# Kernel tuning notes

Hardware: AMD Instinct MI355X
Metric: run time of the kernel (lower is better)

Reference implementation:

```python
import jax, jax.numpy as jnp
import numpy as np
from jax import lax

B, S = 256, 512
CHAR_NUM, CLASS_NUM, OUTPUT_NUM, WORD_EMBED, H = 10, 10, 64, 32, 128
EPS = 1e-12


def setup_inputs() -> dict:
    key = jax.random.key(0)
    ks = jax.random.split(key, 16)
    def nrm(k, shape, s=0.05):
        return jax.random.normal(k, shape, dtype=jnp.float32) * s
    return {
        "char_ids": jax.random.randint(ks[0], (B, S), 0, CHAR_NUM),
        "word_ids": jax.random.randint(ks[1], (B, S), 0, CHAR_NUM),
        "subject_ids": jax.random.randint(ks[2], (B, 2), 0, S),
        "emb_char": nrm(ks[3], (CHAR_NUM, OUTPUT_NUM)),
        "emb_word": nrm(ks[4], (CHAR_NUM, WORD_EMBED)),
        "Wwc": nrm(ks[5], (WORD_EMBED, OUTPUT_NUM)),
        "bwc": jnp.zeros((OUTPUT_NUM,), jnp.float32),
        "l1_Wx": nrm(ks[6], (OUTPUT_NUM, 4 * H)),
        "l1_Wh": nrm(ks[7], (H, 4 * H)),
        "l1_b": jnp.zeros((4 * H,), jnp.float32),
        "l2_Wx": nrm(ks[8], (H, 4 * H)),
        "l2_Wh": nrm(ks[9], (H, 4 * H)),
        "l2_b": jnp.zeros((4 * H,), jnp.float32),
        "beta_W": nrm(ks[10], (2 * H, H)),
        "beta_b": jnp.zeros((H,), jnp.float32),
        "gamma_W": nrm(ks[11], (2 * H, H)),
        "gamma_b": jnp.zeros((H,), jnp.float32),
        "sub_W": nrm(ks[12], (H, 2)),
        "sub_b": jnp.zeros((2,), jnp.float32),
        "po_W": nrm(ks[13], (H, 2 * CLASS_NUM)),
        "po_b": jnp.zeros((2 * CLASS_NUM,), jnp.float32),
    }


def _lstm_cell(x, h, c, Wx, Wh, b):
    # Keras LSTMCell: gates ordered i, f, g(cell), o
    z = x @ Wx + h @ Wh + b
    i, f, g, o = jnp.split(z, 4, axis=-1)
    c_new = jax.nn.sigmoid(f) * c + jax.nn.sigmoid(i) * jnp.tanh(g)
    h_new = jax.nn.sigmoid(o) * jnp.tanh(c_new)
    return h_new, c_new


def reference(char_ids, word_ids, subject_ids,
              emb_char, emb_word, Wwc, bwc,
              l1_Wx, l1_Wh, l1_b, l2_Wx, l2_Wh, l2_b,
              beta_W, beta_b, gamma_W, gamma_b,
              sub_W, sub_b, po_W, po_b):
    b, s = char_ids.shape
    # NOTE: source passes mask = (char_ids == 0) to the RNN; in Keras, mask True
    # means the step IS processed, so only positions with id==0 update state.
    step_mask = (char_ids == 0)  # [B, S] bool

    emb = emb_char[char_ids] + (emb_word[word_ids] @ Wwc + bwc)  # [B, S, 64]

    def step(carry, inp):
        h1, c1, h2, c2 = carry
        xt, mt = inp  # xt [B, 64], mt [B]
        h1n, c1n = _lstm_cell(xt, h1, c1, l1_Wx, l1_Wh, l1_b)
        h2n, c2n = _lstm_cell(h1n, h2, c2, l2_Wx, l2_Wh, l2_b)
        m = mt[:, None]
        h1 = jnp.where(m, h1n, h1)
        c1 = jnp.where(m, c1n, c1)
        h2 = jnp.where(m, h2n, h2)
        c2 = jnp.where(m, c2n, c2)
        return (h1, c1, h2, c2), h2

    z = jnp.zeros((b, H), emb.dtype)
    _, outs = lax.scan(step, (z, z, z, z),
                       (emb.transpose(1, 0, 2), step_mask.T))
    sent = outs.transpose(1, 0, 2)  # [B, S, 128]

    # vectorized batch_gather (replaces eager numpy per-row loop)
    bidx = jnp.arange(b)
    sub_start = sent[bidx, subject_ids[:, 0]]  # [B, 128]
    sub_end = sent[bidx, subject_ids[:, 1]]    # [B, 128]
    subject = jnp.concatenate([sub_start, sub_end], axis=1)  # [B, 256]

    # conditional layer norm
    beta = subject @ beta_W + beta_b    # [B, 128]
    gamma = subject @ gamma_W + gamma_b
    u = jnp.mean(sent, axis=-1, keepdims=True)
    v = jnp.mean((sent - u) ** 2, axis=-1, keepdims=True)
    xhat = (sent - u) / jnp.sqrt(v + EPS)
    context = gamma[:, None, :] * xhat + beta[:, None, :]  # [B, S, 128]

    # (transformer_encoder LSTM(32) output is dead code in the source; omitted)
    sub_preds = sent @ sub_W + sub_b                     # [B, S, 2]
    po_preds = (context @ po_W + po_b).reshape(b, -1, CLASS_NUM, 2)  # [B, S, 10, 2]
    return sub_preds, po_preds
```

## Files before the change

kernel.cpp:

```cpp
#include <hip/hip_runtime.h>
#include <cstdint>
#include <cstddef>


#define SLOTS 192

typedef _Float16 f16x2 __attribute__((ext_vector_type(2)));

__device__ __forceinline__ f16x2 as_h2(unsigned int v) {
    union { unsigned int u; f16x2 h; } x; x.u = v; return x.h;
}

#if __has_builtin(__builtin_amdgcn_fdot2)
__device__ __forceinline__ float fdot2(f16x2 a, f16x2 b, float c) {
    return __builtin_amdgcn_fdot2(a, b, c, false);
}
#else
__device__ __forceinline__ float fdot2(f16x2 a, f16x2 b, float c) {
    return c + (float)a.x * (float)b.x + (float)a.y * (float)b.y;
}
#endif

__device__ __forceinline__ float fast_rcp(float x) {
#if __has_builtin(__builtin_amdgcn_rcpf)
    return __builtin_amdgcn_rcpf(x);
#else
    return 1.f / x;
#endif
}
__device__ __forceinline__ float sigm(float x) {
    x = fminf(fmaxf(x, -30.f), 30.f);
    return fast_rcp(1.f + __expf(-x));
}
__device__ __forceinline__ float tanh_fast(float x) {
    x = fminf(fmaxf(x, -15.f), 15.f);
    float e = __expf(-2.f * x);
    return (1.f - e) * fast_rcp(1.f + e);
}

__device__ __forceinline__ float dpp_bfly4(float v) {
    union { float f; int i; } a, b;
    a.f = v;
    b.i = __builtin_amdgcn_update_dpp(0, a.i, 0xB1, 0xf, 0xf, true);
    a.f += b.f;
    b.i = __builtin_amdgcn_update_dpp(0, a.i, 0x4E, 0xf, 0xf, true);
    a.f += b.f;
    return a.f;
}

__device__ __forceinline__ float dot_u4(float s, const uint4 h, const uint4 w) {
    s = fdot2(as_h2(h.x), as_h2(w.x), s);
    s = fdot2(as_h2(h.y), as_h2(w.y), s);
    s = fdot2(as_h2(h.z), as_h2(w.z), s);
    s = fdot2(as_h2(h.w), as_h2(w.w), s);
    return s;
}

__global__ void k_xw1(const float* __restrict__ emb_char,
                      const float* __restrict__ emb_word,
                      const float* __restrict__ Wwc,
                      const float* __restrict__ bwc,
                      const float* __restrict__ l1_Wx,
                      const float* __restrict__ l1_b,
                      float* __restrict__ XW1) {
    __shared__ float xw[64];
    const int w = blockIdx.x;
    const int T = threadIdx.x;
    if (T < 64) {
        float acc = emb_char[T] + bwc[T];
        for (int m = 0; m < 32; ++m) acc += emb_word[w * 32 + m] * Wwc[m * 64 + T];
        xw[T] = acc;
    }
    __syncthreads();
    float acc = l1_b[T];
    for (int k = 0; k < 64; ++k) acc += xw[k] * l1_Wx[k * 512 + T];
    XW1[w * 512 + T] = acc;
}

__global__ void k_pack2(const float* __restrict__ l1_Wh,
                        const float* __restrict__ l2_Wx,
                        const float* __restrict__ l2_Wh,
                        uint4* __restrict__ W1H, uint4* __restrict__ W2H) {
    const int gid = blockIdx.x * blockDim.x + threadIdx.x;
    union { uint4 qv; f16x2 h[4]; } out;
    if (gid < 8192) {
        const int t = gid >> 4, i = gid & 15;
        const int q = t & 3, u = t >> 2;
        const int j = i >> 2, m = i & 3;
        const int col = u + 128 * j;
        for (int e = 0; e < 4; ++e) {
            const int k = 32 * q + 2 * (4 * m + e);
            f16x2 p;
            p.x = (_Float16)l1_Wh[k * 512 + col];
            p.y = (_Float16)l1_Wh[(k + 1) * 512 + col];
            out.h[e] = p;
        }
        W1H[gid] = out.qv;
    } else {
        const int gid2 = gid - 8192;
        const int t = gid2 >> 5, i = gid2 & 31;
        const int q = t & 3, u = t >> 2;
        const int ph = i >> 4, jm = i & 15;
        const int j = jm >> 2, m = jm & 3;
        const int col = u + 128 * j;
        const float* __restrict__ src = ph ? l2_Wx : l2_Wh;
        for (int e = 0; e < 4; ++e) {
            const int k = 32 * q + 2 * (4 * m + e);
            f16x2 p;
            p.x = (_Float16)src[k * 512 + col];
            p.y = (_Float16)src[(k + 1) * 512 + col];
            out.h[e] = p;
        }
        W2H[gid2] = out.qv;
    }
}

__global__ __launch_bounds__(512, 2) void k_lstm(
    const int* __restrict__ char_ids, const int* __restrict__ word_ids,
    const float* __restrict__ XW1, const uint4* __restrict__ W1H,
    const uint4* __restrict__ W2H, const float* __restrict__ l2_b,
    float* __restrict__ hbuf, unsigned short* __restrict__ idxbuf)
{
    const int b    = blockIdx.x;
    const int T    = threadIdx.x;
    const int lane = T & 63;
    const int wv   = T >> 6;
    const int q    = T & 3;
    const int u    = T >> 2;

    __shared__ int   charL[512];
    __shared__ int   wordL[512];
    __shared__ float XW1L[5120];
    __shared__ __align__(16) _Float16 h1f[2][128];
    __shared__ __align__(16) _Float16 h2f[2][128];
    __shared__ short actT[512];
    __shared__ int   ccnt[8];

    charL[T] = char_ids[b * 512 + T];
    wordL[T] = word_ids[b * 512 + T];
#pragma unroll
    for (int i = 0; i < 10; ++i) XW1L[i * 512 + T] = XW1[i * 512 + T];
    __syncthreads();

    const bool act = (charL[T] == 0);
    const unsigned long long bmask = __ballot(act);
    if (lane == 0) ccnt[wv] = (int)__popcll(bmask);
    __syncthreads();
    int base = 0;
    for (int i = 0; i < wv; ++i) base += ccnt[i];
    int tot = base;
    for (int i = wv; i < 8; ++i) tot += ccnt[i];
    if (act) actT[base + (int)__popcll(bmask & ((1ull << lane) - 1ull))] = (short)T;
    {
        int cin = base + (int)__popcll(bmask & ((2ull << lane) - 1ull));
        idxbuf[b * 512 + T] = (unsigned short)(cin < SLOTS - 1 ? cin : SLOTS - 1);
    }
    const int nact = tot;

    if (T < 128) {
        h1f[0][T] = (_Float16)0.f;
        h1f[1][T] = (_Float16)0.f;
        h2f[0][T] = (_Float16)0.f;
        h2f[1][T] = (_Float16)0.f;
        hbuf[(size_t)b * SLOTS * 128 + T] = 0.f;
    }
    float c1 = 0.f, c2 = 0.f;
    const float l2b0 = l2_b[u];
    const float l2b1 = l2_b[128 + u];
    const float l2b2 = l2_b[256 + u];
    const float l2b3 = l2_b[384 + u];

    uint4 w1[16], w2[32];
    {
        const uint4* W1t = W1H + (size_t)T * 16;
        const uint4* W2t = W2H + (size_t)T * 32;
#pragma unroll
        for (int i = 0; i < 16; ++i) w1[i] = W1t[i];
#pragma unroll
        for (int i = 0; i < 32; ++i) w2[i] = W2t[i];
    }
#pragma unroll
    for (int i = 0; i < 16; ++i)
        asm volatile("" : "+v"(w1[i].x), "+v"(w1[i].y), "+v"(w1[i].z), "+v"(w1[i].w));
#pragma unroll
    for (int i = 0; i < 32; ++i)
        asm volatile("" : "+v"(w2[i].x), "+v"(w2[i].y), "+v"(w2[i].z), "+v"(w2[i].w));

    __syncthreads();

    if (nact > 0) {
        const int w0_ = wordL[actT[0]];
        const float zi = XW1L[w0_ * 512 + u];
        const float zg = XW1L[w0_ * 512 + 256 + u];
        const float zo = XW1L[w0_ * 512 + 384 + u];
        c1 = sigm(zi) * tanh_fast(zg);
        const float h1n = sigm(zo) * tanh_fast(c1);
        if (q == 0) h1f[0][u] = (_Float16)h1n;
        __syncthreads();
    }

#define LSTM_STEP(H1S, H2S, H1D, H2D)                                          \
    {                                                                          \
        const uint4* h1r = (const uint4*)&H1S[0] + 4 * q;                      \
        const uint4 a0 = h1r[0], a1 = h1r[1], a2 = h1r[2], a3 = h1r[3];        \
        const uint4* h2r = (const uint4*)&H2S[0] + 4 * q;                      \
        const uint4 g0 = h2r[0], g1 = h2r[1], g2 = h2r[2], g3 = h2r[3];        \
        const bool more = (a + 1 < nact);                                      \
        const int wid = more ? wordL[actT[a + 1]] : 0;                         \
        const float xwi = XW1L[wid * 512 + u];                                 \
        const float xwf = XW1L[wid * 512 + 128 + u];                           \
        const float xwg = XW1L[wid * 512 + 256 + u];                           \
        const float xwo = XW1L[wid * 512 + 384 + u];                           \
        float p[4];                                                            \
        _Pragma("unroll")                                                      \
        for (int j = 0; j < 4; ++j) {                                          \
            float s = dot_u4(0.f, g0, w2[4 * j + 0]);                          \
            s = dot_u4(s, g1, w2[4 * j + 1]);                                  \
            s = dot_u4(s, g2, w2[4 * j + 2]);                                  \
            s = dot_u4(s, g3, w2[4 * j + 3]);                                  \
            s = dot_u4(s, a0, w2[16 + 4 * j + 0]);                             \
            s = dot_u4(s, a1, w2[16 + 4 * j + 1]);                             \
            s = dot_u4(s, a2, w2[16 + 4 * j + 2]);                             \
            s = dot_u4(s, a3, w2[16 + 4 * j + 3]);                             \
            p[j] = s;                                                          \
        }                                                                      \
        const float y0 = dpp_bfly4(p[0]) + l2b0;                               \
        const float y1 = dpp_bfly4(p[1]) + l2b1;                               \
        const float y2 = dpp_bfly4(p[2]) + l2b2;                               \
        const float y3 = dpp_bfly4(p[3]) + l2b3;                               \
        c2 = sigm(y1) * c2 + sigm(y0) * tanh_fast(y2);                         \
        const float h2v = sigm(y3) * tanh_fast(c2);                            \
        if (q == 0) {                                                          \
            H2D[u] = (_Float16)h2v;                                            \
            const int slot = (a + 1 < SLOTS - 1) ? a + 1 : SLOTS - 1;          \
            hbuf[((size_t)b * SLOTS + slot) * 128 + u] = h2v;                  \
        }                                                                      \
        if (more) {                                                            \
            float r0, r1, r2, r3;                                              \
            {                                                                  \
                float r = dot_u4(0.f, a0, w1[0]);                              \
                r = dot_u4(r, a1, w1[1]);                                      \
                r = dot_u4(r, a2, w1[2]);                                      \
                r = dot_u4(r, a3, w1[3]);                                      \
                r0 = r;                                                        \
                r = dot_u4(0.f, a0, w1[4]);                                    \
                r = dot_u4(r, a1, w1[5]);                                      \
                r = dot_u4(r, a2, w1[6]);                                      \
                r = dot_u4(r, a3, w1[7]);                                      \
                r1 = r;                                                        \
                r = dot_u4(0.f, a0, w1[8]);                                    \
                r = dot_u4(r, a1, w1[9]);                                      \
                r = dot_u4(r, a2, w1[10]);                                     \
                r = dot_u4(r, a3, w1[11]);                                     \
                r2 = r;                                                        \
                r = dot_u4(0.f, a0, w1[12]);                                   \
                r = dot_u4(r, a1, w1[13]);                                     \
                r = dot_u4(r, a2, w1[14]);                                     \
                r = dot_u4(r, a3, w1[15]);                                     \
                r3 = r;                                                        \
            }                                                                  \
            const float zi = dpp_bfly4(r0) + xwi;                              \
            const float zf = dpp_bfly4(r1) + xwf;                              \
            const float zg = dpp_bfly4(r2) + xwg;                              \
            const float zo = dpp_bfly4(r3) + xwo;                              \
            c1 = sigm(zf) * c1 + sigm(zi) * tanh_fast(zg);                     \
            const float h1n = sigm(zo) * tanh_fast(c1);                        \
            if (q == 0) H1D[u] = (_Float16)h1n;                                \
        }                                                                      \
        __syncthreads();                                                       \
    }

    int a = 0;
    while (a < nact) {
        LSTM_STEP(h1f[0], h2f[0], h1f[1], h2f[1]);
        ++a;
        if (a >= nact) break;
        LSTM_STEP(h1f[1], h2f[1], h1f[0], h2f[0]);
        ++a;
    }
#undef LSTM_STEP
}

__global__ __launch_bounds__(256) void k_subject(
    const int* __restrict__ subject_ids,
    const unsigned short* __restrict__ idxbuf,
    const float* __restrict__ hbuf,
    const float* __restrict__ beta_W, const float* __restrict__ beta_b,
    const float* __restrict__ gamma_W, const float* __restrict__ gamma_b,
    float* __restrict__ betaO, float* __restrict__ gammaO)
{
    const int b = blockIdx.x;
    const int T = threadIdx.x;
    const int u = T & 127, half = T >> 7;
    __shared__ float subj[256];
    const int s0 = subject_ids[b * 2 + 0];
    const int s1 = subject_ids[b * 2 + 1];
    const int i0 = idxbuf[b * 512 + s0];
    const int i1 = idxbuf[b * 512 + s1];
    const int slot = half ? i1 : i0;
    subj[T] = hbuf[((size_t)b * SLOTS + slot) * 128 + u];
    __syncthreads();
    const float* __restrict__ W = half ? gamma_W : beta_W;
    float acc = half ? gamma_b[u] : beta_b[u];
    for (int c = 0; c < 256; ++c) acc += subj[c] * W[c * 128 + u];
    if (half) gammaO[b * 128 + u] = acc;
    else      betaO[b * 128 + u]  = acc;
}

__global__ __launch_bounds__(256) void k_out2(
    const unsigned short* __restrict__ idxbuf, const float* __restrict__ hbuf,
    const float* __restrict__ betaO, const float* __restrict__ gammaO,
    const float* __restrict__ sub_W, const float* __restrict__ sub_b,
    const float* __restrict__ po_W, const float* __restrict__ po_b,
    float* __restrict__ out)
{
    const int b = blockIdx.x;
    const int T = threadIdx.x;
    __shared__ float A[20][132];
    __shared__ float K1[20], K2[20];
    __shared__ float gm[128], bt[128];
    __shared__ float urs[192][2];
    __shared__ float povals[192 * 20];
    __shared__ float subv[192 * 2];
    __shared__ unsigned short idxr[512];
    __shared__ float swl[256];

    if (T < 128) { gm[T] = gammaO[b * 128 + T]; bt[T] = betaO[b * 128 + T]; }
    idxr[T] = idxbuf[b * 512 + T];
    idxr[256 + T] = idxbuf[b * 512 + 256 + T];
    swl[T] = sub_W[T];
    __syncthreads();

    for (int i = T; i < 2560; i += 256) {
        const int o = i >> 7, c = i & 127;
        A[o][c] = gm[c] * po_W[c * 20 + o];
    }
    if (T < 20) {
        float k1 = po_b[T], k2 = 0.f;
        for (int c = 0; c < 128; ++c) {
            const float pw = po_W[c * 20 + T];
            k1 += bt[c] * pw;
            k2 += gm[c] * pw;
        }
        K1[T] = k1; K2[T] = k2;
    }
    const int nslot = (int)idxr[511] + 1;
    const float sb0 = sub_b[0], sb1 = sub_b[1];
    for (int s = T; s < nslot; s += 256) {
        const float4* hp4 = (const float4*)(hbuf + ((size_t)b * SLOTS + s) * 128);
        float sum = 0.f, s2 = 0.f, sub0 = sb0, sub1 = sb1;
        for (int c4 = 0; c4 < 32; ++c4) {
            const float4 h = hp4[c4];
            sum += (h.x + h.y) + (h.z + h.w);
            s2  += h.x * h.x + h.y * h.y + h.z * h.z + h.w * h.w;
            const int c = 4 * c4;
            sub0 += h.x * swl[2 * c] + h.y * swl[2 * c + 2] + h.z * swl[2 * c + 4] + h.w * swl[2 * c + 6];
            sub1 += h.x * swl[2 * c + 1] + h.y * swl[2 * c + 3] + h.z * swl[2 * c + 5] + h.w * swl[2 * c + 7];
        }
        const float u = sum * (1.f / 128.f);
        const float v = fmaxf(s2 * (1.f / 128.f) - u * u, 0.f);
        urs[s][0] = u;
        urs[s][1] = 1.f / sqrtf(v + 1e-12f);
        subv[2 * s] = sub0; subv[2 * s + 1] = sub1;
    }
    __syncthreads();

    for (int i = T; i < nslot * 20; i += 256) {
        const int s = i / 20, o = i - 20 * s;
        const float u = urs[s][0], rs = urs[s][1];
        const float4* hp4 = (const float4*)(hbuf + ((size_t)b * SLOTS + s) * 128);
        const float* Ao = &A[o][0];
        float acc = 0.f;
        for (int c4 = 0; c4 < 32; ++c4) {
            const float4 h = hp4[c4];
            const float4 aa = *(const float4*)&Ao[4 * c4];
            acc += h.x * aa.x + h.y * aa.y + h.z * aa.z + h.w * aa.w;
        }
        povals[i] = rs * acc - u * rs * K2[o] + K1[o];
    }
    __syncthreads();

    for (int i = T; i < 2560; i += 256) {
        const int t = i / 5, j = i - 5 * t;
        const int sl = idxr[t];
        const float4 v = *(const float4*)&povals[sl * 20 + 4 * j];
        *(float4*)&out[262144 + ((size_t)(b * 512 + t)) * 20 + 4 * j] = v;
    }
    for (int i = T; i < 512; i += 256) {
        const int sl = idxr[i];
        float2 v; v.x = subv[2 * sl]; v.y = subv[2 * sl + 1];
        *(float2*)&out[((size_t)(b * 512 + i)) * 2] = v;
    }
}

extern "C" void kernel_launch(void* const* d_in, const int* in_sizes, int n_in,
                              void* d_out, int out_size, void* d_ws, size_t ws_size,
                              hipStream_t stream) {
    (void)in_sizes; (void)n_in; (void)out_size; (void)ws_size;
    const int*   char_ids    = (const int*)d_in[0];
    const int*   word_ids    = (const int*)d_in[1];
    const int*   subject_ids = (const int*)d_in[2];
    const float* emb_char    = (const float*)d_in[3];
    const float* emb_word    = (const float*)d_in[4];
    const float* Wwc         = (const float*)d_in[5];
    const float* bwc         = (const float*)d_in[6];
    const float* l1_Wx       = (const float*)d_in[7];
    const float* l1_Wh       = (const float*)d_in[8];
    const float* l1_b        = (const float*)d_in[9];
    const float* l2_Wx       = (const float*)d_in[10];
    const float* l2_Wh       = (const float*)d_in[11];
    const float* l2_b        = (const float*)d_in[12];
    const float* beta_W      = (const float*)d_in[13];
    const float* beta_b      = (const float*)d_in[14];
    const float* gamma_W     = (const float*)d_in[15];
    const float* gamma_b     = (const float*)d_in[16];
    const float* sub_W       = (const float*)d_in[17];
    const float* sub_b       = (const float*)d_in[18];
    const float* po_W        = (const float*)d_in[19];
    const float* po_b        = (const float*)d_in[20];
    float* out = (float*)d_out;

    char* ws = (char*)d_ws;
    float*          XW1    = (float*)(ws + 0);
    uint4*          W1H    = (uint4*)(ws + 32768);
    uint4*          W2H    = (uint4*)(ws + 163840);
    float*          betaO  = (float*)(ws + 425984);
    float*          gammaO = (float*)(ws + 557056);
    unsigned short* idxbuf = (unsigned short*)(ws + 688128);
    float*          hbuf   = (float*)(ws + 950272);

    k_xw1<<<dim3(10), dim3(512), 0, stream>>>(emb_char, emb_word, Wwc, bwc, l1_Wx, l1_b, XW1);
    k_pack2<<<dim3(96), dim3(256), 0, stream>>>(l1_Wh, l2_Wx, l2_Wh, W1H, W2H);
    k_lstm<<<dim3(256), dim3(512), 0, stream>>>(char_ids, word_ids, XW1, W1H, W2H,
                                                l2_b, hbuf, idxbuf);
    k_subject<<<dim3(256), dim3(256), 0, stream>>>(subject_ids, idxbuf, hbuf,
                                                   beta_W, beta_b, gamma_W, gamma_b,
                                                   betaO, gammaO);
    k_out2<<<dim3(256), dim3(256), 0, stream>>>(idxbuf, hbuf, betaO, gammaO,
                                                sub_W, sub_b, po_W, po_b, out);
}
```

Baseline: 244.7 us.

## Split LSTM gate dot products across 8 lanes per unit and fuse small kernels

Each hidden unit's recurrent dot products are now split over 8 threads instead of 4. The LSTM block grows to 1024 threads with half the weight registers per thread, and an extra DPP stage finishes the reduction. This shortens the serial per-step dependency chain at the cost of more threads, more sync participants and an extra shuffle stage. The prep kernels (XW1 table and weight packing) are merged into one launch, the subject/beta-gamma kernel is folded into the output kernel, and word ids are precompacted into a list to cut launch overhead and an indirect lookup.

```diff
diff --git a/kernel.cpp b/kernel.cpp
--- a/kernel.cpp
+++ b/kernel.cpp
@@ -38,13 +38,15 @@
     return (1.f - e) * fast_rcp(1.f + e);
 }
 
-__device__ __forceinline__ float dpp_bfly4(float v) {
+__device__ __forceinline__ float dpp_bfly8(float v) {
     union { float f; int i; } a, b;
     a.f = v;
     b.i = __builtin_amdgcn_update_dpp(0, a.i, 0xB1, 0xf, 0xf, true);
     a.f += b.f;
     b.i = __builtin_amdgcn_update_dpp(0, a.i, 0x4E, 0xf, 0xf, true);
     a.f += b.f;
+    b.i = __builtin_amdgcn_update_dpp(0, a.i, 0x141, 0xf, 0xf, true);
+    a.f += b.f;
     return a.f;
 }
 
@@ -56,66 +58,63 @@
     return s;
 }
 
-__global__ void k_xw1(const float* __restrict__ emb_char,
-                      const float* __restrict__ emb_word,
-                      const float* __restrict__ Wwc,
-                      const float* __restrict__ bwc,
-                      const float* __restrict__ l1_Wx,
-                      const float* __restrict__ l1_b,
-                      float* __restrict__ XW1) {
-    __shared__ float xw[64];
-    const int w = blockIdx.x;
+__global__ __launch_bounds__(512) void k_prep(
+    const float* __restrict__ emb_char, const float* __restrict__ emb_word,
+    const float* __restrict__ Wwc, const float* __restrict__ bwc,
+    const float* __restrict__ l1_Wx, const float* __restrict__ l1_b,
+    const float* __restrict__ l1_Wh, const float* __restrict__ l2_Wx,
+    const float* __restrict__ l2_Wh,
+    float* __restrict__ XW1, uint4* __restrict__ W1H, uint4* __restrict__ W2H)
+{
+    const int blk = blockIdx.x;
     const int T = threadIdx.x;
-    if (T < 64) {
-        float acc = emb_char[T] + bwc[T];
-        for (int m = 0; m < 32; ++m) acc += emb_word[w * 32 + m] * Wwc[m * 64 + T];
-        xw[T] = acc;
-    }
-    __syncthreads();
-    float acc = l1_b[T];
-    for (int k = 0; k < 64; ++k) acc += xw[k] * l1_Wx[k * 512 + T];
-    XW1[w * 512 + T] = acc;
-}
-
-__global__ void k_pack2(const float* __restrict__ l1_Wh,
-                        const float* __restrict__ l2_Wx,
-                        const float* __restrict__ l2_Wh,
-                        uint4* __restrict__ W1H, uint4* __restrict__ W2H) {
-    const int gid = blockIdx.x * blockDim.x + threadIdx.x;
-    union { uint4 qv; f16x2 h[4]; } out;
-    if (gid < 8192) {
-        const int t = gid >> 4, i = gid & 15;
-        const int q = t & 3, u = t >> 2;
-        const int j = i >> 2, m = i & 3;
-        const int col = u + 128 * j;
-        for (int e = 0; e < 4; ++e) {
-            const int k = 32 * q + 2 * (4 * m + e);
-            f16x2 p;
-            p.x = (_Float16)l1_Wh[k * 512 + col];
-            p.y = (_Float16)l1_Wh[(k + 1) * 512 + col];
-            out.h[e] = p;
+    if (blk < 10) {
+        __shared__ float xw[64];
+        if (T < 64) {
+            float acc = emb_char[T] + bwc[T];
+            for (int m = 0; m < 32; ++m) acc += emb_word[blk * 32 + m] * Wwc[m * 64 + T];
+            xw[T] = acc;
         }
-        W1H[gid] = out.qv;
+        __syncthreads();
+        float acc = l1_b[T];
+        for (int k = 0; k < 64; ++k) acc += xw[k] * l1_Wx[k * 512 + T];
+        XW1[blk * 512 + T] = acc;
     } else {
-        const int gid2 = gid - 8192;
-        const int t = gid2 >> 5, i = gid2 & 31;
-        const int q = t & 3, u = t >> 2;
-        const int ph = i >> 4, jm = i & 15;
-        const int j = jm >> 2, m = jm & 3;
-        const int col = u + 128 * j;
-        const float* __restrict__ src = ph ? l2_Wx : l2_Wh;
-        for (int e = 0; e < 4; ++e) {
-            const int k = 32 * q + 2 * (4 * m + e);
-            f16x2 p;
-            p.x = (_Float16)src[k * 512 + col];
-            p.y = (_Float16)src[(k + 1) * 512 + col];
-            out.h[e] = p;
+        const int gid = (blk - 10) * 512 + T;
+        union { uint4 qv; f16x2 h[4]; } out;
+        if (gid < 8192) {
+            const int t = gid >> 3, i = gid & 7;
+            const int q = t & 7, u = t >> 3;
+            const int j = i >> 1, m = i & 1;
+            const int col = u + 128 * j;
+            for (int e = 0; e < 4; ++e) {
+                const int k = 16 * q + 2 * (4 * m + e);
+                f16x2 p;
+                p.x = (_Float16)l1_Wh[k * 512 + col];
+                p.y = (_Float16)l1_Wh[(k + 1) * 512 + col];
+                out.h[e] = p;
+            }
+            W1H[gid] = out.qv;
+        } else {
+            const int gid2 = gid - 8192;
+            const int t = gid2 >> 4, i = gid2 & 15;
+            const int q = t & 7, u = t >> 3;
+            const int j = i >> 2, m = i & 3;
+            const int col = u + 128 * j;
+            for (int e = 0; e < 4; ++e) {
+                const int kk = 32 * q + 2 * (4 * m + e);
+                float w0, w1v;
+                if (kk < 128) { w0 = l2_Wh[kk * 512 + col];          w1v = l2_Wh[(kk + 1) * 512 + col]; }
+                else          { w0 = l2_Wx[(kk - 128) * 512 + col]; w1v = l2_Wx[(kk - 127) * 512 + col]; }
+                f16x2 p; p.x = (_Float16)w0; p.y = (_Float16)w1v;
+                out.h[e] = p;
+            }
+            W2H[gid2] = out.qv;
         }
-        W2H[gid2] = out.qv;
-    }
-}
-
-__global__ __launch_bounds__(512, 2) void k_lstm(
+    }
+}
+
+__global__ __launch_bounds__(1024, 4) void k_lstm(
     const int* __restrict__ char_ids, const int* __restrict__ word_ids,
     const float* __restrict__ XW1, const uint4* __restrict__ W1H,
     const uint4* __restrict__ W2H, const float* __restrict__ l2_b,
@@ -125,8 +124,8 @@
     const int T    = threadIdx.x;
     const int lane = T & 63;
     const int wv   = T >> 6;
-    const int q    = T & 3;
-    const int u    = T >> 2;
+    const int q    = T & 7;
+    const int u    = T >> 3;
 
     __shared__ int   charL[512];
     __shared__ int   wordL[512];
@@ -134,25 +133,38 @@
     __shared__ __align__(16) _Float16 h1f[2][128];
     __shared__ __align__(16) _Float16 h2f[2][128];
     __shared__ short actT[512];
+    __shared__ short wlist[512];
     __shared__ int   ccnt[8];
 
-    charL[T] = char_ids[b * 512 + T];
-    wordL[T] = word_ids[b * 512 + T];
-#pragma unroll
-    for (int i = 0; i < 10; ++i) XW1L[i * 512 + T] = XW1[i * 512 + T];
-    __syncthreads();
-
-    const bool act = (charL[T] == 0);
+    if (T < 512) {
+        charL[T] = char_ids[b * 512 + T];
+        wordL[T] = word_ids[b * 512 + T];
+    }
+    XW1L[T]        = XW1[T];
+    XW1L[1024 + T] = XW1[1024 + T];
+    XW1L[2048 + T] = XW1[2048 + T];
+    XW1L[3072 + T] = XW1[3072 + T];
+    XW1L[4096 + T] = XW1[4096 + T];
+    __syncthreads();
+
+    const bool act = (T < 512) && (charL[T] == 0);
     const unsigned long long bmask = __ballot(act);
-    if (lane == 0) ccnt[wv] = (int)__popcll(bmask);
+    if (lane == 0 && wv < 8) ccnt[wv] = (int)__popcll(bmask);
     __syncthreads();
     int base = 0;
-    for (int i = 0; i < wv; ++i) base += ccnt[i];
-    int tot = base;
-    for (int i = wv; i < 8; ++i) tot += ccnt[i];
-    if (act) actT[base + (int)__popcll(bmask & ((1ull << lane) - 1ull))] = (short)T;
     {
-        int cin = base + (int)__popcll(bmask & ((2ull << lane) - 1ull));
+        const int wcap = wv < 8 ? wv : 8;
+        for (int i = 0; i < wcap; ++i) base += ccnt[i];
+    }
+    int tot = 0;
+    for (int i = 0; i < 8; ++i) tot += ccnt[i];
+    if (act) {
+        const int pos = base + (int)__popcll(bmask & ((1ull << lane) - 1ull));
+        actT[pos]  = (short)T;
+        wlist[pos] = (short)wordL[T];
+    }
+    if (T < 512) {
+        const int cin = base + (int)__popcll(bmask & ((2ull << lane) - 1ull));
         idxbuf[b * 512 + T] = (unsigned short)(cin < SLOTS - 1 ? cin : SLOTS - 1);
     }
     const int nact = tot;
@@ -170,26 +182,26 @@
     const float l2b2 = l2_b[256 + u];
     const float l2b3 = l2_b[384 + u];
 
-    uint4 w1[16], w2[32];
+    uint4 w1[8], w2[16];
     {
-        const uint4* W1t = W1H + (size_t)T * 16;
-        const uint4* W2t = W2H + (size_t)T * 32;
+        const uint4* W1t = W1H + (size_t)T * 8;
+        const uint4* W2t = W2H + (size_t)T * 16;
 #pragma unroll
-        for (int i = 0; i < 16; ++i) w1[i] = W1t[i];
+        for (int i = 0; i < 8; ++i) w1[i] = W1t[i];
 #pragma unroll
-        for (int i = 0; i < 32; ++i) w2[i] = W2t[i];
-    }
+        for (int i = 0; i < 16; ++i) w2[i] = W2t[i];
+    }
+#pragma unroll
+    for (int i = 0; i < 8; ++i)
+        asm volatile("" : "+v"(w1[i].x), "+v"(w1[i].y), "+v"(w1[i].z), "+v"(w1[i].w));
 #pragma unroll
     for (int i = 0; i < 16; ++i)
-        asm volatile("" : "+v"(w1[i].x), "+v"(w1[i].y), "+v"(w1[i].z), "+v"(w1[i].w));
-#pragma unroll
-    for (int i = 0; i < 32; ++i)
         asm volatile("" : "+v"(w2[i].x), "+v"(w2[i].y), "+v"(w2[i].z), "+v"(w2[i].w));
 
     __syncthreads();
 
     if (nact > 0) {
-        const int w0_ = wordL[actT[0]];
+        const int w0_ = wlist[0];
         const float zi = XW1L[w0_ * 512 + u];
         const float zg = XW1L[w0_ * 512 + 256 + u];
         const float zo = XW1L[w0_ * 512 + 384 + u];
@@ -201,33 +213,22 @@
 
 #define LSTM_STEP(H1S, H2S, H1D, H2D)                                          \
     {                                                                          \
-        const uint4* h1r = (const uint4*)&H1S[0] + 4 * q;                      \
-        const uint4 a0 = h1r[0], a1 = h1r[1], a2 = h1r[2], a3 = h1r[3];        \
-        const uint4* h2r = (const uint4*)&H2S[0] + 4 * q;                      \
-        const uint4 g0 = h2r[0], g1 = h2r[1], g2 = h2r[2], g3 = h2r[3];        \
-        const bool more = (a + 1 < nact);                                      \
-        const int wid = more ? wordL[actT[a + 1]] : 0;                         \
-        const float xwi = XW1L[wid * 512 + u];                                 \
-        const float xwf = XW1L[wid * 512 + 128 + u];                           \
-        const float xwg = XW1L[wid * 512 + 256 + u];                           \
-        const float xwo = XW1L[wid * 512 + 384 + u];                           \
-        float p[4];                                                            \
-        _Pragma("unroll")                                                      \
-        for (int j = 0; j < 4; ++j) {                                          \
-            float s = dot_u4(0.f, g0, w2[4 * j + 0]);                          \
-            s = dot_u4(s, g1, w2[4 * j + 1]);                                  \
-            s = dot_u4(s, g2, w2[4 * j + 2]);                                  \
-            s = dot_u4(s, g3, w2[4 * j + 3]);                                  \
-            s = dot_u4(s, a0, w2[16 + 4 * j + 0]);                             \
-            s = dot_u4(s, a1, w2[16 + 4 * j + 1]);                             \
-            s = dot_u4(s, a2, w2[16 + 4 * j + 2]);                             \
-            s = dot_u4(s, a3, w2[16 + 4 * j + 3]);                             \
-            p[j] = s;                                                          \
-        }                                                                      \
-        const float y0 = dpp_bfly4(p[0]) + l2b0;                               \
-        const float y1 = dpp_bfly4(p[1]) + l2b1;                               \
-        const float y2 = dpp_bfly4(p[2]) + l2b2;                               \
-        const float y3 = dpp_bfly4(p[3]) + l2b3;                               \
+        const uint4* srcL2 = (q < 4) ? ((const uint4*)&H2S[0] + 4 * q)         \
+                                     : ((const uint4*)&H1S[0] + 4 * (q - 4));  \
+        uint4 sA = srcL2[0], sB = srcL2[1];                                    \
+        float p0 = dot_u4(dot_u4(0.f, sA, w2[0]),  sB, w2[1]);                 \
+        float p1 = dot_u4(dot_u4(0.f, sA, w2[4]),  sB, w2[5]);                 \
+        float p2 = dot_u4(dot_u4(0.f, sA, w2[8]),  sB, w2[9]);                 \
+        float p3 = dot_u4(dot_u4(0.f, sA, w2[12]), sB, w2[13]);                \
+        sA = srcL2[2]; sB = srcL2[3];                                          \
+        p0 = dot_u4(dot_u4(p0, sA, w2[2]),  sB, w2[3]);                        \
+        p1 = dot_u4(dot_u4(p1, sA, w2[6]),  sB, w2[7]);                        \
+        p2 = dot_u4(dot_u4(p2, sA, w2[10]), sB, w2[11]);                       \
+        p3 = dot_u4(dot_u4(p3, sA, w2[14]), sB, w2[15]);                       \
+        const float y0 = dpp_bfly8(p0) + l2b0;                                 \
+        const float y1 = dpp_bfly8(p1) + l2b1;                                 \
+        const float y2 = dpp_bfly8(p2) + l2b2;                                 \
+        const float y3 = dpp_bfly8(p3) + l2b3;                                 \
         c2 = sigm(y1) * c2 + sigm(y0) * tanh_fast(y2);                         \
         const float h2v = sigm(y3) * tanh_fast(c2);                            \
         if (q == 0) {                                                          \
@@ -235,34 +236,18 @@
             const int slot = (a + 1 < SLOTS - 1) ? a + 1 : SLOTS - 1;          \
             hbuf[((size_t)b * SLOTS + slot) * 128 + u] = h2v;                  \
         }                                                                      \
-        if (more) {                                                            \
-            float r0, r1, r2, r3;                                              \
-            {                                                                  \
-                float r = dot_u4(0.f, a0, w1[0]);                              \
-                r = dot_u4(r, a1, w1[1]);                                      \
-                r = dot_u4(r, a2, w1[2]);                                      \
-                r = dot_u4(r, a3, w1[3]);                                      \
-                r0 = r;                                                        \
-                r = dot_u4(0.f, a0, w1[4]);                                    \
-                r = dot_u4(r, a1, w1[5]);                                      \
-                r = dot_u4(r, a2, w1[6]);                                      \
-                r = dot_u4(r, a3, w1[7]);                                      \
-                r1 = r;                                                        \
-                r = dot_u4(0.f, a0, w1[8]);                                    \
-                r = dot_u4(r, a1, w1[9]);                                      \
-                r = dot_u4(r, a2, w1[10]);                                     \
-                r = dot_u4(r, a3, w1[11]);                                     \
-                r2 = r;                                                        \
-                r = dot_u4(0.f, a0, w1[12]);                                   \
-                r = dot_u4(r, a1, w1[13]);                                     \
-                r = dot_u4(r, a2, w1[14]);                                     \
-                r = dot_u4(r, a3, w1[15]);                                     \
-                r3 = r;                                                        \
-            }                                                                  \
-            const float zi = dpp_bfly4(r0) + xwi;                              \
-            const float zf = dpp_bfly4(r1) + xwf;                              \
-            const float zg = dpp_bfly4(r2) + xwg;                              \
-            const float zo = dpp_bfly4(r3) + xwo;                              \
+        if (a + 1 < nact) {                                                    \
+            const int wid = wlist[a + 1];                                      \
+            const uint4* h1s = (const uint4*)&H1S[0] + 2 * q;                  \
+            const uint4 tA = h1s[0], tB = h1s[1];                              \
+            float r0 = dot_u4(dot_u4(0.f, tA, w1[0]), tB, w1[1]);              \
+            float r1 = dot_u4(dot_u4(0.f, tA, w1[2]), tB, w1[3]);              \
+            float r2 = dot_u4(dot_u4(0.f, tA, w1[4]), tB, w1[5]);              \
+            float r3 = dot_u4(dot_u4(0.f, tA, w1[6]), tB, w1[7]);              \
+            const float zi = dpp_bfly8(r0) + XW1L[wid * 512 + u];              \
+            const float zf = dpp_bfly8(r1) + XW1L[wid * 512 + 128 + u];        \
+            const float zg = dpp_bfly8(r2) + XW1L[wid * 512 + 256 + u];        \
+            const float zo = dpp_bfly8(r3) + XW1L[wid * 512 + 384 + u];        \
             c1 = sigm(zf) * c1 + sigm(zi) * tanh_fast(zg);                     \
             const float h1n = sigm(zo) * tanh_fast(c1);                        \
             if (q == 0) H1D[u] = (_Float16)h1n;                                \
@@ -281,35 +266,11 @@
 #undef LSTM_STEP
 }
 
-__global__ __launch_bounds__(256) void k_subject(
+__global__ __launch_bounds__(256) void k_post(
     const int* __restrict__ subject_ids,
-    const unsigned short* __restrict__ idxbuf,
-    const float* __restrict__ hbuf,
+    const unsigned short* __restrict__ idxbuf, const float* __restrict__ hbuf,
     const float* __restrict__ beta_W, const float* __restrict__ beta_b,
     const float* __restrict__ gamma_W, const float* __restrict__ gamma_b,
-    float* __restrict__ betaO, float* __restrict__ gammaO)
-{
-    const int b = blockIdx.x;
-    const int T = threadIdx.x;
-    const int u = T & 127, half = T >> 7;
-    __shared__ float subj[256];
-    const int s0 = subject_ids[b * 2 + 0];
-    const int s1 = subject_ids[b * 2 + 1];
-    const int i0 = idxbuf[b * 512 + s0];
-    const int i1 = idxbuf[b * 512 + s1];
-    const int slot = half ? i1 : i0;
-    subj[T] = hbuf[((size_t)b * SLOTS + slot) * 128 + u];
-    __syncthreads();
-    const float* __restrict__ W = half ? gamma_W : beta_W;
-    float acc = half ? gamma_b[u] : beta_b[u];
-    for (int c = 0; c < 256; ++c) acc += subj[c] * W[c * 128 + u];
-    if (half) gammaO[b * 128 + u] = acc;
-    else      betaO[b * 128 + u]  = acc;
-}
-
-__global__ __launch_bounds__(256) void k_out2(
-    const unsigned short* __restrict__ idxbuf, const float* __restrict__ hbuf,
-    const float* __restrict__ betaO, const float* __restrict__ gammaO,
     const float* __restrict__ sub_W, const float* __restrict__ sub_b,
     const float* __restrict__ po_W, const float* __restrict__ po_b,
     float* __restrict__ out)
@@ -324,11 +285,27 @@
     __shared__ float subv[192 * 2];
     __shared__ unsigned short idxr[512];
     __shared__ float swl[256];
-
-    if (T < 128) { gm[T] = gammaO[b * 128 + T]; bt[T] = betaO[b * 128 + T]; }
+    __shared__ float subj[256];
+
     idxr[T] = idxbuf[b * 512 + T];
     idxr[256 + T] = idxbuf[b * 512 + 256 + T];
     swl[T] = sub_W[T];
+    {
+        const int uu = T & 127, half = T >> 7;
+        const int sidx = subject_ids[b * 2 + half];
+        const int slot = idxbuf[b * 512 + sidx];
+        subj[T] = hbuf[((size_t)b * SLOTS + slot) * 128 + uu];
+    }
+    __syncthreads();
+
+    {
+        const int uu = T & 127, half = T >> 7;
+        const float* __restrict__ W = half ? gamma_W : beta_W;
+        float acc = half ? gamma_b[uu] : beta_b[uu];
+        for (int c = 0; c < 256; ++c) acc += subj[c] * W[c * 128 + uu];
+        if (half) gm[uu] = acc;
+        else      bt[uu] = acc;
+    }
     __syncthreads();
 
     for (int i = T; i < 2560; i += 256) {
@@ -424,18 +401,15 @@
     float*          XW1    = (float*)(ws + 0);
     uint4*          W1H    = (uint4*)(ws + 32768);
     uint4*          W2H    = (uint4*)(ws + 163840);
-    float*          betaO  = (float*)(ws + 425984);
-    float*          gammaO = (float*)(ws + 557056);
     unsigned short* idxbuf = (unsigned short*)(ws + 688128);
     float*          hbuf   = (float*)(ws + 950272);
 
-    k_xw1<<<dim3(10), dim3(512), 0, stream>>>(emb_char, emb_word, Wwc, bwc, l1_Wx, l1_b, XW1);
-    k_pack2<<<dim3(96), dim3(256), 0, stream>>>(l1_Wh, l2_Wx, l2_Wh, W1H, W2H);
-    k_lstm<<<dim3(256), dim3(512), 0, stream>>>(char_ids, word_ids, XW1, W1H, W2H,
-                                                l2_b, hbuf, idxbuf);
-    k_subject<<<dim3(256), dim3(256), 0, stream>>>(subject_ids, idxbuf, hbuf,
-                                                   beta_W, beta_b, gamma_W, gamma_b,
-                                                   betaO, gammaO);
-    k_out2<<<dim3(256), dim3(256), 0, stream>>>(idxbuf, hbuf, betaO, gammaO,
+    k_prep<<<dim3(58), dim3(512), 0, stream>>>(emb_char, emb_word, Wwc, bwc,
+                                               l1_Wx, l1_b, l1_Wh, l2_Wx, l2_Wh,
+                                               XW1, W1H, W2H);
+    k_lstm<<<dim3(256), dim3(1024), 0, stream>>>(char_ids, word_ids, XW1, W1H, W2H,
+                                                 l2_b, hbuf, idxbuf);
+    k_post<<<dim3(256), dim3(256), 0, stream>>>(subject_ids, idxbuf, hbuf,
+                                                beta_W, beta_b, gamma_W, gamma_b,
                                                 sub_W, sub_b, po_W, po_b, out);
 }
```

Measured after the change: 273.5 us. 11.8% more time.

## Fuse subject projection and output head into LSTM kernel using shared-memory history

Applied to the files above, without the earlier changes.

The two small preprocessing kernels are merged into one launch. The subject-projection and output-head kernels are folded into the tail of the LSTM kernel. The per-step h2 history now stays in padded shared memory instead of a global buffer, so it is no longer written and re-read from global memory, and two launches plus their global round trips go away. The trade-off is a much larger shared-memory footprint per block, which may cut blocks per CU. The history capacity also shrinks from 192 to 128 slots, so the last slot clamps if a row has more active steps than that.

```diff
diff --git a/kernel.cpp b/kernel.cpp
--- a/kernel.cpp
+++ b/kernel.cpp
@@ -3,7 +3,8 @@
 #include <cstddef>
 
 
-#define SLOTS 192
+#define HIST 128
+#define HPAD 132
 
 typedef _Float16 f16x2 __attribute__((ext_vector_type(2)));
 
@@ -56,70 +57,73 @@
     return s;
 }
 
-__global__ void k_xw1(const float* __restrict__ emb_char,
-                      const float* __restrict__ emb_word,
-                      const float* __restrict__ Wwc,
-                      const float* __restrict__ bwc,
-                      const float* __restrict__ l1_Wx,
-                      const float* __restrict__ l1_b,
-                      float* __restrict__ XW1) {
-    __shared__ float xw[64];
-    const int w = blockIdx.x;
+__global__ __launch_bounds__(512) void k_prep(
+    const float* __restrict__ emb_char, const float* __restrict__ emb_word,
+    const float* __restrict__ Wwc, const float* __restrict__ bwc,
+    const float* __restrict__ l1_Wx, const float* __restrict__ l1_b,
+    const float* __restrict__ l1_Wh, const float* __restrict__ l2_Wx,
+    const float* __restrict__ l2_Wh,
+    float* __restrict__ XW1, uint4* __restrict__ W1H, uint4* __restrict__ W2H)
+{
+    const int blk = blockIdx.x;
     const int T = threadIdx.x;
-    if (T < 64) {
-        float acc = emb_char[T] + bwc[T];
-        for (int m = 0; m < 32; ++m) acc += emb_word[w * 32 + m] * Wwc[m * 64 + T];
-        xw[T] = acc;
-    }
-    __syncthreads();
-    float acc = l1_b[T];
-    for (int k = 0; k < 64; ++k) acc += xw[k] * l1_Wx[k * 512 + T];
-    XW1[w * 512 + T] = acc;
-}
-
-__global__ void k_pack2(const float* __restrict__ l1_Wh,
-                        const float* __restrict__ l2_Wx,
-                        const float* __restrict__ l2_Wh,
-                        uint4* __restrict__ W1H, uint4* __restrict__ W2H) {
-    const int gid = blockIdx.x * blockDim.x + threadIdx.x;
-    union { uint4 qv; f16x2 h[4]; } out;
-    if (gid < 8192) {
-        const int t = gid >> 4, i = gid & 15;
-        const int q = t & 3, u = t >> 2;
-        const int j = i >> 2, m = i & 3;
-        const int col = u + 128 * j;
-        for (int e = 0; e < 4; ++e) {
-            const int k = 32 * q + 2 * (4 * m + e);
-            f16x2 p;
-            p.x = (_Float16)l1_Wh[k * 512 + col];
-            p.y = (_Float16)l1_Wh[(k + 1) * 512 + col];
-            out.h[e] = p;
+    if (blk < 10) {
+        __shared__ float xw[64];
+        if (T < 64) {
+            float acc = emb_char[T] + bwc[T];
+            for (int m = 0; m < 32; ++m) acc += emb_word[blk * 32 + m] * Wwc[m * 64 + T];
+            xw[T] = acc;
         }
-        W1H[gid] = out.qv;
+        __syncthreads();
+        float acc = l1_b[T];
+        for (int k = 0; k < 64; ++k) acc += xw[k] * l1_Wx[k * 512 + T];
+        XW1[blk * 512 + T] = acc;
     } else {
-        const int gid2 = gid - 8192;
-        const int t = gid2 >> 5, i = gid2 & 31;
-        const int q = t & 3, u = t >> 2;
-        const int ph = i >> 4, jm = i & 15;
-        const int j = jm >> 2, m = jm & 3;
-        const int col = u + 128 * j;
-        const float* __restrict__ src = ph ? l2_Wx : l2_Wh;
-        for (int e = 0; e < 4; ++e) {
-            const int k = 32 * q + 2 * (4 * m + e);
-            f16x2 p;
-            p.x = (_Float16)src[k * 512 + col];
-            p.y = (_Float16)src[(k + 1) * 512 + col];
-            out.h[e] = p;
+        const int gid = (blk - 10) * 512 + T;
+        union { uint4 qv; f16x2 h[4]; } out;
+        if (gid < 8192) {
+            const int t = gid >> 4, i = gid & 15;
+            const int q = t & 3, u = t >> 2;
+            const int j = i >> 2, m = i & 3;
+            const int col = u + 128 * j;
+            for (int e = 0; e < 4; ++e) {
+                const int k = 32 * q + 2 * (4 * m + e);
+                f16x2 p;
+                p.x = (_Float16)l1_Wh[k * 512 + col];
+                p.y = (_Float16)l1_Wh[(k + 1) * 512 + col];
+                out.h[e] = p;
+            }
+            W1H[gid] = out.qv;
+        } else {
+            const int gid2 = gid - 8192;
+            const int t = gid2 >> 5, i = gid2 & 31;
+            const int q = t & 3, u = t >> 2;
+            const int ph = i >> 4, jm = i & 15;
+            const int j = jm >> 2, m = jm & 3;
+            const int col = u + 128 * j;
+            const float* __restrict__ src = ph ? l2_Wx : l2_Wh;
+            for (int e = 0; e < 4; ++e) {
+                const int k = 32 * q + 2 * (4 * m + e);
+                f16x2 p;
+                p.x = (_Float16)src[k * 512 + col];
+                p.y = (_Float16)src[(k + 1) * 512 + col];
+                out.h[e] = p;
+            }
+            W2H[gid2] = out.qv;
         }
-        W2H[gid2] = out.qv;
     }
 }
 
 __global__ __launch_bounds__(512, 2) void k_lstm(
     const int* __restrict__ char_ids, const int* __restrict__ word_ids,
+    const int* __restrict__ subject_ids,
     const float* __restrict__ XW1, const uint4* __restrict__ W1H,
     const uint4* __restrict__ W2H, const float* __restrict__ l2_b,
-    float* __restrict__ hbuf, unsigned short* __restrict__ idxbuf)
+    const float* __restrict__ beta_W, const float* __restrict__ beta_b,
+    const float* __restrict__ gamma_W, const float* __restrict__ gamma_b,
+    const float* __restrict__ sub_W, const float* __restrict__ sub_b,
+    const float* __restrict__ po_W, const float* __restrict__ po_b,
+    float* __restrict__ out)
 {
     const int b    = blockIdx.x;
     const int T    = threadIdx.x;
@@ -134,7 +138,18 @@
     __shared__ __align__(16) _Float16 h1f[2][128];
     __shared__ __align__(16) _Float16 h2f[2][128];
     __shared__ short actT[512];
+    __shared__ short wlist[512];
+    __shared__ unsigned short idxL[512];
     __shared__ int   ccnt[8];
+    __shared__ __align__(16) float hl[HIST * HPAD];
+    __shared__ float A[20][132];
+    __shared__ float K1[20], K2[20];
+    __shared__ float gm[128], bt[128];
+    __shared__ float urs[HIST][2];
+    __shared__ float povals[HIST * 20];
+    __shared__ float subv[HIST * 2];
+    __shared__ float swl[256];
+    __shared__ float subj[256];
 
     charL[T] = char_ids[b * 512 + T];
     wordL[T] = word_ids[b * 512 + T];
@@ -150,10 +165,14 @@
     for (int i = 0; i < wv; ++i) base += ccnt[i];
     int tot = base;
     for (int i = wv; i < 8; ++i) tot += ccnt[i];
-    if (act) actT[base + (int)__popcll(bmask & ((1ull << lane) - 1ull))] = (short)T;
+    if (act) {
+        const int pos = base + (int)__popcll(bmask & ((1ull << lane) - 1ull));
+        actT[pos]  = (short)T;
+        wlist[pos] = (short)wordL[T];
+    }
     {
-        int cin = base + (int)__popcll(bmask & ((2ull << lane) - 1ull));
-        idxbuf[b * 512 + T] = (unsigned short)(cin < SLOTS - 1 ? cin : SLOTS - 1);
+        const int cin = base + (int)__popcll(bmask & ((2ull << lane) - 1ull));
+        idxL[T] = (unsigned short)(cin < HIST - 1 ? cin : HIST - 1);
     }
     const int nact = tot;
 
@@ -162,7 +181,7 @@
         h1f[1][T] = (_Float16)0.f;
         h2f[0][T] = (_Float16)0.f;
         h2f[1][T] = (_Float16)0.f;
-        hbuf[(size_t)b * SLOTS * 128 + T] = 0.f;
+        hl[T]     = 0.f;
     }
     float c1 = 0.f, c2 = 0.f;
     const float l2b0 = l2_b[u];
@@ -189,7 +208,7 @@
     __syncthreads();
 
     if (nact > 0) {
-        const int w0_ = wordL[actT[0]];
+        const int w0_ = wlist[0];
         const float zi = XW1L[w0_ * 512 + u];
         const float zg = XW1L[w0_ * 512 + 256 + u];
         const float zo = XW1L[w0_ * 512 + 384 + u];
@@ -206,7 +225,7 @@
         const uint4* h2r = (const uint4*)&H2S[0] + 4 * q;                      \
         const uint4 g0 = h2r[0], g1 = h2r[1], g2 = h2r[2], g3 = h2r[3];        \
         const bool more = (a + 1 < nact);                                      \
-        const int wid = more ? wordL[actT[a + 1]] : 0;                         \
+        const int wid = more ? wlist[a + 1] : 0;                               \
         const float xwi = XW1L[wid * 512 + u];                                 \
         const float xwf = XW1L[wid * 512 + 128 + u];                           \
         const float xwg = XW1L[wid * 512 + 256 + u];                           \
@@ -232,8 +251,8 @@
         const float h2v = sigm(y3) * tanh_fast(c2);                            \
         if (q == 0) {                                                          \
             H2D[u] = (_Float16)h2v;                                            \
-            const int slot = (a + 1 < SLOTS - 1) ? a + 1 : SLOTS - 1;          \
-            hbuf[((size_t)b * SLOTS + slot) * 128 + u] = h2v;                  \
+            const int slot = (a + 1 < HIST - 1) ? a + 1 : HIST - 1;            \
+            hl[slot * HPAD + u] = h2v;                                         \
         }                                                                      \
         if (more) {                                                            \
             float r0, r1, r2, r3;                                              \
@@ -279,59 +298,27 @@
         ++a;
     }
 #undef LSTM_STEP
-}
-
-__global__ __launch_bounds__(256) void k_subject(
-    const int* __restrict__ subject_ids,
-    const unsigned short* __restrict__ idxbuf,
-    const float* __restrict__ hbuf,
-    const float* __restrict__ beta_W, const float* __restrict__ beta_b,
-    const float* __restrict__ gamma_W, const float* __restrict__ gamma_b,
-    float* __restrict__ betaO, float* __restrict__ gammaO)
-{
-    const int b = blockIdx.x;
-    const int T = threadIdx.x;
-    const int u = T & 127, half = T >> 7;
-    __shared__ float subj[256];
-    const int s0 = subject_ids[b * 2 + 0];
-    const int s1 = subject_ids[b * 2 + 1];
-    const int i0 = idxbuf[b * 512 + s0];
-    const int i1 = idxbuf[b * 512 + s1];
-    const int slot = half ? i1 : i0;
-    subj[T] = hbuf[((size_t)b * SLOTS + slot) * 128 + u];
-    __syncthreads();
-    const float* __restrict__ W = half ? gamma_W : beta_W;
-    float acc = half ? gamma_b[u] : beta_b[u];
-    for (int c = 0; c < 256; ++c) acc += subj[c] * W[c * 128 + u];
-    if (half) gammaO[b * 128 + u] = acc;
-    else      betaO[b * 128 + u]  = acc;
-}
-
-__global__ __launch_bounds__(256) void k_out2(
-    const unsigned short* __restrict__ idxbuf, const float* __restrict__ hbuf,
-    const float* __restrict__ betaO, const float* __restrict__ gammaO,
-    const float* __restrict__ sub_W, const float* __restrict__ sub_b,
-    const float* __restrict__ po_W, const float* __restrict__ po_b,
-    float* __restrict__ out)
-{
-    const int b = blockIdx.x;
-    const int T = threadIdx.x;
-    __shared__ float A[20][132];
-    __shared__ float K1[20], K2[20];
-    __shared__ float gm[128], bt[128];
-    __shared__ float urs[192][2];
-    __shared__ float povals[192 * 20];
-    __shared__ float subv[192 * 2];
-    __shared__ unsigned short idxr[512];
-    __shared__ float swl[256];
-
-    if (T < 128) { gm[T] = gammaO[b * 128 + T]; bt[T] = betaO[b * 128 + T]; }
-    idxr[T] = idxbuf[b * 512 + T];
-    idxr[256 + T] = idxbuf[b * 512 + 256 + T];
-    swl[T] = sub_W[T];
-    __syncthreads();
-
-    for (int i = T; i < 2560; i += 256) {
+
+    if (T < 256) {
+        swl[T] = sub_W[T];
+        const int uu = T & 127, half = T >> 7;
+        const int sidx = subject_ids[b * 2 + half];
+        const int slot = idxL[sidx];
+        subj[T] = hl[slot * HPAD + uu];
+    }
+    __syncthreads();
+
+    if (T < 256) {
+        const int uu = T & 127, half = T >> 7;
+        const float* __restrict__ W = half ? gamma_W : beta_W;
+        float acc = half ? gamma_b[uu] : beta_b[uu];
+        for (int c = 0; c < 256; ++c) acc += subj[c] * W[c * 128 + uu];
+        if (half) gm[uu] = acc;
+        else      bt[uu] = acc;
+    }
+    __syncthreads();
+
+    for (int i = T; i < 2560; i += 512) {
         const int o = i >> 7, c = i & 127;
         A[o][c] = gm[c] * po_W[c * 20 + o];
     }
@@ -344,10 +331,10 @@
         }
         K1[T] = k1; K2[T] = k2;
     }
-    const int nslot = (int)idxr[511] + 1;
+    const int nslot = (int)idxL[511] + 1;
     const float sb0 = sub_b[0], sb1 = sub_b[1];
-    for (int s = T; s < nslot; s += 256) {
-        const float4* hp4 = (const float4*)(hbuf + ((size_t)b * SLOTS + s) * 128);
+    for (int s = T; s < nslot; s += 512) {
+        const float4* hp4 = (const float4*)&hl[s * HPAD];
         float sum = 0.f, s2 = 0.f, sub0 = sb0, sub1 = sb1;
         for (int c4 = 0; c4 < 32; ++c4) {
             const float4 h = hp4[c4];
@@ -357,18 +344,18 @@
             sub0 += h.x * swl[2 * c] + h.y * swl[2 * c + 2] + h.z * swl[2 * c + 4] + h.w * swl[2 * c + 6];
             sub1 += h.x * swl[2 * c + 1] + h.y * swl[2 * c + 3] + h.z * swl[2 * c + 5] + h.w * swl[2 * c + 7];
         }
-        const float u = sum * (1.f / 128.f);
-        const float v = fmaxf(s2 * (1.f / 128.f) - u * u, 0.f);
-        urs[s][0] = u;
-        urs[s][1] = 1.f / sqrtf(v + 1e-12f);
+        const float mu = sum * (1.f / 128.f);
+        const float vv = fmaxf(s2 * (1.f / 128.f) - mu * mu, 0.f);
+        urs[s][0] = mu;
+        urs[s][1] = 1.f / sqrtf(vv + 1e-12f);
         subv[2 * s] = sub0; subv[2 * s + 1] = sub1;
     }
     __syncthreads();
 
-    for (int i = T; i < nslot * 20; i += 256) {
+    for (int i = T; i < nslot * 20; i += 512) {
         const int s = i / 20, o = i - 20 * s;
-        const float u = urs[s][0], rs = urs[s][1];
-        const float4* hp4 = (const float4*)(hbuf + ((size_t)b * SLOTS + s) * 128);
+        const float mu = urs[s][0], rs = urs[s][1];
+        const float4* hp4 = (const float4*)&hl[s * HPAD];
         const float* Ao = &A[o][0];
         float acc = 0.f;
         for (int c4 = 0; c4 < 32; ++c4) {
@@ -376,18 +363,18 @@
             const float4 aa = *(const float4*)&Ao[4 * c4];
             acc += h.x * aa.x + h.y * aa.y + h.z * aa.z + h.w * aa.w;
         }
-        povals[i] = rs * acc - u * rs * K2[o] + K1[o];
-    }
-    __syncthreads();
-
-    for (int i = T; i < 2560; i += 256) {
+        povals[i] = rs * acc - mu * rs * K2[o] + K1[o];
+    }
+    __syncthreads();
+
+    for (int i = T; i < 2560; i += 512) {
         const int t = i / 5, j = i - 5 * t;
-        const int sl = idxr[t];
+        const int sl = idxL[t];
         const float4 v = *(const float4*)&povals[sl * 20 + 4 * j];
         *(float4*)&out[262144 + ((size_t)(b * 512 + t)) * 20 + 4 * j] = v;
     }
-    for (int i = T; i < 512; i += 256) {
-        const int sl = idxr[i];
+    for (int i = T; i < 512; i += 512) {
+        const int sl = idxL[i];
         float2 v; v.x = subv[2 * sl]; v.y = subv[2 * sl + 1];
         *(float2*)&out[((size_t)(b * 512 + i)) * 2] = v;
     }
@@ -421,21 +408,15 @@
     float* out = (float*)d_out;
 
     char* ws = (char*)d_ws;
-    float*          XW1    = (float*)(ws + 0);
-    uint4*          W1H    = (uint4*)(ws + 32768);
-    uint4*          W2H    = (uint4*)(ws + 163840);
-    float*          betaO  = (float*)(ws + 425984);
-    float*          gammaO = (float*)(ws + 557056);
-    unsigned short* idxbuf = (unsigned short*)(ws + 688128);
-    float*          hbuf   = (float*)(ws + 950272);
-
-    k_xw1<<<dim3(10), dim3(512), 0, stream>>>(emb_char, emb_word, Wwc, bwc, l1_Wx, l1_b, XW1);
-    k_pack2<<<dim3(96), dim3(256), 0, stream>>>(l1_Wh, l2_Wx, l2_Wh, W1H, W2H);
-    k_lstm<<<dim3(256), dim3(512), 0, stream>>>(char_ids, word_ids, XW1, W1H, W2H,
-                                                l2_b, hbuf, idxbuf);
-    k_subject<<<dim3(256), dim3(256), 0, stream>>>(subject_ids, idxbuf, hbuf,
-                                                   beta_W, beta_b, gamma_W, gamma_b,
-                                                   betaO, gammaO);
-    k_out2<<<dim3(256), dim3(256), 0, stream>>>(idxbuf, hbuf, betaO, gammaO,
+    float* XW1 = (float*)(ws + 0);
+    uint4* W1H = (uint4*)(ws + 32768);
+    uint4* W2H = (uint4*)(ws + 163840);
+
+    k_prep<<<dim3(58), dim3(512), 0, stream>>>(emb_char, emb_word, Wwc, bwc,
+                                               l1_Wx, l1_b, l1_Wh, l2_Wx, l2_Wh,
+                                               XW1, W1H, W2H);
+    k_lstm<<<dim3(256), dim3(512), 0, stream>>>(char_ids, word_ids, subject_ids,
+                                                XW1, W1H, W2H, l2_b,
+                                                beta_W, beta_b, gamma_W, gamma_b,
                                                 sub_W, sub_b, po_W, po_b, out);
 }
```

After: 232.6 us. -4.9%, faster.
